# Kernel tuning notes

Hardware: AMD Instinct MI355X
Metric: run time of the kernel (lower is better)

The kernel has to match this reference:

```python
import jax, jax.numpy as jnp
import numpy as np

B, M, FIN, FOUT = 8, 2048, 256, 128
ALPHA = 0.2  # LeakyReLU negative slope
NEG_INF = -9e15


def _xavier_uniform(key, shape, gain):
    fan_in, fan_out = shape[0], shape[1]
    bound = gain * np.sqrt(6.0 / (fan_in + fan_out))
    return jax.random.uniform(key, shape, jnp.float32, -bound, bound)


def setup_inputs() -> dict:
    key = jax.random.key(0)
    k1, k2, k3, k4 = jax.random.split(key, 4)
    x = jax.random.normal(k1, (B, M, FIN), jnp.float32)
    adj1 = jax.random.randint(k2, (B, M, M), 0, 2).astype(jnp.int32)
    W = _xavier_uniform(k3, (FIN, FOUT), gain=2.0)
    a = _xavier_uniform(k4, (2 * FOUT, 1), gain=2.0)
    return {"input": x, "adj1": adj1, "W": W, "a": a}


def reference(input, adj1, W, a):
    # h: [B, M, FOUT]
    h = jnp.matmul(input, W)
    # e[b,i,j] = leakyrelu( concat(h_i, h_j) . a ) = leakyrelu( h_i.a1 + h_j.a2 )
    a1 = a[:FOUT, 0]   # [FOUT]
    a2 = a[FOUT:, 0]   # [FOUT]
    f1 = jnp.einsum('bme,e->bm', h, a1)  # source (row i) term
    f2 = jnp.einsum('bme,e->bm', h, a2)  # target (col j) term
    e = jax.nn.leaky_relu(f1[:, :, None] + f2[:, None, :], negative_slope=ALPHA)  # [B,M,M]
    scores = jnp.where(adj1 > 0, e, NEG_INF)
    attention = jax.nn.softmax(scores, axis=-1)
    # dropout is identity in eval mode (training=False)
    h_prime = jnp.matmul(attention, h)  # [B,M,FOUT]
    return jax.nn.elu(h_prime)  # concat=True branch
```

## Files before the change

### kernel.cpp

```cpp
#include <hip/hip_runtime.h>
#include <math.h>

#define B_    8
#define M_    2048
#define FIN_  256
#define FOUT_ 128
#define ALPHA_ 0.2f
#define NEG_INF_ -9.0e15f

typedef unsigned short u16;
typedef __attribute__((ext_vector_type(8))) short bf16x8;
typedef __attribute__((ext_vector_type(4))) float f32x4;

static __device__ __forceinline__ u16 f2bf(float f) {
  union { float f; unsigned u; } v; v.f = f;
  unsigned r = v.u + 0x7FFFu + ((v.u >> 16) & 1u);
  return (u16)(r >> 16);
}

__global__ __launch_bounds__(256) void k_wt(const float* __restrict__ W,
                                            u16* __restrict__ Wt) {
  const int id = blockIdx.x * 256 + threadIdx.x;
  const int f = id >> 8;
  const int k = id & 255;
  Wt[f * FIN_ + k] = f2bf(W[(size_t)k * FOUT_ + f]);
}

__global__ __launch_bounds__(128) void k_xw(const float* __restrict__ x,
                                            const u16* __restrict__ Wt,
                                            const float* __restrict__ a,
                                            u16* __restrict__ ht,
                                            float* __restrict__ f1,
                                            float* __restrict__ f2) {
  int blk = blockIdx.x;
  blk = (blk & 7) * 128 + (blk >> 3);
  const int b    = blk >> 7;
  const int row0 = (blk & 127) * 16;
  const int rowg = b * M_ + row0;
  const int tid  = threadIdx.x;
  const int w  = tid >> 6;
  const int l  = tid & 63;
  const int lr = l & 15;
  const int g  = l >> 4;
  const int fbase = w * 64;

  f32x4 acc[4];
#pragma unroll
  for (int ft = 0; ft < 4; ++ft) acc[ft] = (f32x4){0.f, 0.f, 0.f, 0.f};

  const float* xr = x + (size_t)(rowg + lr) * FIN_;
#pragma unroll
  for (int ks = 0; ks < 8; ++ks) {
    float4 xa = *(const float4*)(xr + ks * 32 + g * 8);
    float4 xc = *(const float4*)(xr + ks * 32 + g * 8 + 4);
    bf16x8 af;
    af[0] = (short)f2bf(xa.x); af[1] = (short)f2bf(xa.y);
    af[2] = (short)f2bf(xa.z); af[3] = (short)f2bf(xa.w);
    af[4] = (short)f2bf(xc.x); af[5] = (short)f2bf(xc.y);
    af[6] = (short)f2bf(xc.z); af[7] = (short)f2bf(xc.w);
#pragma unroll
    for (int ft = 0; ft < 4; ++ft) {
      bf16x8 bf = *(const bf16x8*)(Wt + (fbase + ft * 16 + lr) * FIN_ + ks * 32 + g * 8);
      acc[ft] = __builtin_amdgcn_mfma_f32_16x16x32_bf16(af, bf, acc[ft], 0, 0, 0);
    }
  }

  __shared__ float sf1[2][16], sf2[2][16];
  float v1[4] = {0.f, 0.f, 0.f, 0.f};
  float v2[4] = {0.f, 0.f, 0.f, 0.f};
#pragma unroll
  for (int ft = 0; ft < 4; ++ft) {
    const float a1v = a[fbase + ft * 16 + lr];
    const float a2v = a[FOUT_ + fbase + ft * 16 + lr];
#pragma unroll
    for (int j = 0; j < 4; ++j) {
      v1[j] += acc[ft][j] * a1v;
      v2[j] += acc[ft][j] * a2v;
    }
  }
#pragma unroll
  for (int off = 1; off < 16; off <<= 1) {
#pragma unroll
    for (int j = 0; j < 4; ++j) {
      v1[j] += __shfl_xor(v1[j], off);
      v2[j] += __shfl_xor(v2[j], off);
    }
  }
  if (lr == 0) {
#pragma unroll
    for (int j = 0; j < 4; ++j) {
      sf1[w][g * 4 + j] = v1[j];
      sf2[w][g * 4 + j] = v2[j];
    }
  }

  __shared__ float hs[16][132];
#pragma unroll
  for (int ft = 0; ft < 4; ++ft)
#pragma unroll
    for (int j = 0; j < 4; ++j)
      hs[g * 4 + j][fbase + ft * 16 + lr] = acc[ft][j];
  __syncthreads();

  if (tid < 16) {
    f1[rowg + tid] = sf1[0][tid] + sf1[1][tid];
    f2[rowg + tid] = sf2[0][tid] + sf2[1][tid];
  }
  const int f = tid;
  union { u16 u[16]; uint4 q[2]; } hb;
#pragma unroll
  for (int i = 0; i < 16; ++i) hb.u[i] = f2bf(hs[i][f]);
  u16* dst = ht + (size_t)(b * FOUT_ + f) * M_ + row0;
  *(uint4*)(dst)     = hb.q[0];
  *(uint4*)(dst + 8) = hb.q[1];
}

__global__ __launch_bounds__(256) void k_attn(const u16* __restrict__ ht,
                                              const int* __restrict__ adj,
                                              const float* __restrict__ f1,
                                              const float* __restrict__ f2,
                                              float* __restrict__ out) {
  int blk = blockIdx.x;
  blk = (blk & 7) * 128 + (blk >> 3);
  const int b    = blk >> 7;
  const int row0 = (blk & 127) * 16;
  const int tid = threadIdx.x;
  const int w  = tid >> 6;
  const int l  = tid & 63;
  const int lr = l & 15;
  const int g  = l >> 4;
  const int r  = tid >> 4;
  const int ts = tid & 15;

  __shared__ __align__(16) u16 P[2][16][128];
  __shared__ float sscale[2][16];
  __shared__ float smx[16], ssum[16], f1s[16];

  if (tid < 16) {
    smx[tid]  = -INFINITY;
    ssum[tid] = 0.f;
    f1s[tid]  = f1[b * M_ + row0 + tid];
  }

  f32x4 acc0 = (f32x4){0.f, 0.f, 0.f, 0.f};
  f32x4 acc1 = (f32x4){0.f, 0.f, 0.f, 0.f};

  const int fbase = w * 32;
  const int* ap   = adj + ((size_t)b * M_ + row0 + r) * M_ + ts * 8;
  const float* fp = f2 + b * M_ + ts * 8;
  const u16* hp0  = ht + (size_t)(b * FOUT_ + fbase + lr) * M_ + g * 8;
  const u16* hp1  = hp0 + 16 * M_;
  char* Pb = (char*)P;

  int4   ajA = *(const int4*)(ap);
  int4   ajB = *(const int4*)(ap + 4);
  float4 fvA = *(const float4*)(fp);
  float4 fvB = *(const float4*)(fp + 4);
  bf16x8 vbuf0[8], vbuf1[8];
#pragma unroll
  for (int ks = 0; ks < 4; ++ks) {
    vbuf0[ks]     = *(const bf16x8*)(hp0 + ks * 32);
    vbuf0[4 + ks] = *(const bf16x8*)(hp1 + ks * 32);
  }

  __syncthreads();

  auto iter = [&](int it, bf16x8 (&vcur)[8], bf16x8 (&vnxt)[8]) {
    const int n0 = it * 128;
    const int bi = it & 1;
    const int   aj[8] = {ajA.x, ajA.y, ajA.z, ajA.w, ajB.x, ajB.y, ajB.z, ajB.w};
    const float fv[8] = {fvA.x, fvA.y, fvA.z, fvA.w, fvB.x, fvB.y, fvB.z, fvB.w};
    const float f1r = f1s[r];
    float s[8];
#pragma unroll
    for (int i = 0; i < 8; ++i) {
      float z = f1r + fv[i];
      float e = z > 0.f ? z : ALPHA_ * z;
      s[i] = aj[i] > 0 ? e : NEG_INF_;
    }
    float cmax = s[0];
#pragma unroll
    for (int i = 1; i < 8; ++i) cmax = fmaxf(cmax, s[i]);
#pragma unroll
    for (int off = 1; off < 16; off <<= 1) cmax = fmaxf(cmax, __shfl_xor(cmax, off));
    const float m_old = smx[r];
    const float m_new = fmaxf(m_old, cmax);
    const float scl   = __expf(m_old - m_new);
    float psum = 0.f;
#pragma unroll
    for (int i = 0; i < 8; ++i) {
      float p = __expf(s[i] - m_new);
      s[i] = p;
      psum += p;
    }
#pragma unroll
    for (int off = 1; off < 16; off <<= 1) psum += __shfl_xor(psum, off);
    if (ts == 0) {
      smx[r]       = m_new;
      ssum[r]      = ssum[r] * scl + psum;
      sscale[bi][r] = scl;
    }
    union { u16 u[8]; uint4 q; } pw;
#pragma unroll
    for (int i = 0; i < 8; ++i) pw.u[i] = f2bf(s[i]);
    *(uint4*)(Pb + bi * 4096 + r * 256 + ((ts ^ (r & 7)) << 4)) = pw.q;
    __syncthreads();

    const int nn = (it + 1 < 16) ? (n0 + 128) : 0;
    ajA = *(const int4*)(ap + nn);
    ajB = *(const int4*)(ap + nn + 4);
    fvA = *(const float4*)(fp + nn);
    fvB = *(const float4*)(fp + nn + 4);
#pragma unroll
    for (int ks = 0; ks < 4; ++ks) {
      vnxt[ks]     = *(const bf16x8*)(hp0 + nn + ks * 32);
      vnxt[4 + ks] = *(const bf16x8*)(hp1 + nn + ks * 32);
    }
    f32x4 scv = { sscale[bi][g * 4],     sscale[bi][g * 4 + 1],
                  sscale[bi][g * 4 + 2], sscale[bi][g * 4 + 3] };
    acc0 *= scv;
    acc1 *= scv;
#pragma unroll
    for (int ks = 0; ks < 4; ++ks) {
      bf16x8 af = *(const bf16x8*)(Pb + bi * 4096 + lr * 256 +
                                   (((ks * 4 + g) ^ (lr & 7)) << 4));
      acc0 = __builtin_amdgcn_mfma_f32_16x16x32_bf16(af, vcur[ks],     acc0, 0, 0, 0);
      acc1 = __builtin_amdgcn_mfma_f32_16x16x32_bf16(af, vcur[4 + ks], acc1, 0, 0, 0);
    }
  };

#pragma unroll 1
  for (int it = 0; it < 16; it += 2) {
    iter(it,     vbuf0, vbuf1);
    iter(it + 1, vbuf1, vbuf0);
  }

  f32x4 inv = { 1.f / ssum[g * 4], 1.f / ssum[g * 4 + 1],
                1.f / ssum[g * 4 + 2], 1.f / ssum[g * 4 + 3] };
#pragma unroll
  for (int j = 0; j < 4; ++j) {
    const size_t orow = ((size_t)b * M_ + row0 + g * 4 + j) * FOUT_;
    float t0 = acc0[j] * inv[j];
    float t1 = acc1[j] * inv[j];
    out[orow + fbase + lr]      = t0 > 0.f ? t0 : __expf(t0) - 1.f;
    out[orow + fbase + 16 + lr] = t1 > 0.f ? t1 : __expf(t1) - 1.f;
  }
}

extern "C" void kernel_launch(void* const* d_in, const int* in_sizes, int n_in,
                              void* d_out, int out_size, void* d_ws, size_t ws_size,
                              hipStream_t stream) {
  const float* x   = (const float*)d_in[0];
  const int*   adj = (const int*)d_in[1];
  const float* W   = (const float*)d_in[2];
  const float* a   = (const float*)d_in[3];
  float* out = (float*)d_out;

  char* ws = (char*)d_ws;
  u16*   Wt = (u16*)ws;
  float* f1 = (float*)(ws + 65536);
  float* f2 = (float*)(ws + 131072);
  u16*   ht = (u16*)(ws + 196608);

  hipLaunchKernelGGL(k_wt,   dim3(128),  dim3(256), 0, stream, W, Wt);
  hipLaunchKernelGGL(k_xw,   dim3(1024), dim3(128), 0, stream, x, Wt, a, ht, f1, f2);
  hipLaunchKernelGGL(k_attn, dim3(1024), dim3(256), 0, stream, ht, adj, f1, f2, out);
}
```

Measured before the change: 259.3 us.

## Pack adjacency into bitmask in a pre-pass and read bits in attention

Adds a k_pack kernel that reads the int32 adjacency matrix once with coalesced loads and ballots each 64-column chunk into a 64-bit mask. The attention kernel then loads one 32-bit word per thread per tile instead of two int4 vectors, and tests bits to build the masked scores. The goal is to shrink the memory traffic and load latency inside the attention main loop. The cost is an extra kernel launch that still streams the full adjacency from memory, so total adjacency bytes read do not drop.

```diff
diff --git a/kernel.cpp b/kernel.cpp
--- a/kernel.cpp
+++ b/kernel.cpp
@@ -9,6 +9,8 @@
 #define NEG_INF_ -9.0e15f
 
 typedef unsigned short u16;
+typedef unsigned int   u32;
+typedef unsigned long long u64;
 typedef __attribute__((ext_vector_type(8))) short bf16x8;
 typedef __attribute__((ext_vector_type(4))) float f32x4;
 
@@ -24,6 +26,23 @@
   const int f = id >> 8;
   const int k = id & 255;
   Wt[f * FIN_ + k] = f2bf(W[(size_t)k * FOUT_ + f]);
+}
+
+__global__ __launch_bounds__(256) void k_pack(const int* __restrict__ adj,
+                                              u64* __restrict__ mask64) {
+  const int wid = (blockIdx.x * 256 + threadIdx.x) >> 6;
+  const int l   = threadIdx.x & 63;
+  const size_t base = (size_t)wid * 4096 + l;
+#pragma unroll 1
+  for (int kk = 0; kk < 4; ++kk) {
+#pragma unroll
+    for (int k = 0; k < 16; ++k) {
+      const int step = kk * 16 + k;
+      int v = adj[base + (size_t)step * 64];
+      u64 bal = __ballot(v > 0);
+      if (l == 0) mask64[(size_t)wid * 64 + step] = bal;
+    }
+  }
 }
 
 __global__ __launch_bounds__(128) void k_xw(const float* __restrict__ x,
@@ -116,7 +135,7 @@
 }
 
 __global__ __launch_bounds__(256) void k_attn(const u16* __restrict__ ht,
-                                              const int* __restrict__ adj,
+                                              const u32* __restrict__ mask32,
                                               const float* __restrict__ f1,
                                               const float* __restrict__ f2,
                                               float* __restrict__ out) {
@@ -146,14 +165,14 @@
   f32x4 acc1 = (f32x4){0.f, 0.f, 0.f, 0.f};
 
   const int fbase = w * 32;
-  const int* ap   = adj + ((size_t)b * M_ + row0 + r) * M_ + ts * 8;
+  const u32* mp   = mask32 + ((size_t)b * M_ + row0 + r) * 64 + (ts >> 2);
+  const int mshift = (ts & 3) * 8;
   const float* fp = f2 + b * M_ + ts * 8;
   const u16* hp0  = ht + (size_t)(b * FOUT_ + fbase + lr) * M_ + g * 8;
   const u16* hp1  = hp0 + 16 * M_;
   char* Pb = (char*)P;
 
-  int4   ajA = *(const int4*)(ap);
-  int4   ajB = *(const int4*)(ap + 4);
+  u32    mwA = mp[0];
   float4 fvA = *(const float4*)(fp);
   float4 fvB = *(const float4*)(fp + 4);
   bf16x8 vbuf0[8], vbuf1[8];
@@ -166,9 +185,8 @@
   __syncthreads();
 
   auto iter = [&](int it, bf16x8 (&vcur)[8], bf16x8 (&vnxt)[8]) {
-    const int n0 = it * 128;
     const int bi = it & 1;
-    const int   aj[8] = {ajA.x, ajA.y, ajA.z, ajA.w, ajB.x, ajB.y, ajB.z, ajB.w};
+    const u32   mbyte = (mwA >> mshift) & 0xffu;
     const float fv[8] = {fvA.x, fvA.y, fvA.z, fvA.w, fvB.x, fvB.y, fvB.z, fvB.w};
     const float f1r = f1s[r];
     float s[8];
@@ -176,7 +194,7 @@
     for (int i = 0; i < 8; ++i) {
       float z = f1r + fv[i];
       float e = z > 0.f ? z : ALPHA_ * z;
-      s[i] = aj[i] > 0 ? e : NEG_INF_;
+      s[i] = (mbyte & (1u << i)) ? e : NEG_INF_;
     }
     float cmax = s[0];
 #pragma unroll
@@ -196,8 +214,8 @@
 #pragma unroll
     for (int off = 1; off < 16; off <<= 1) psum += __shfl_xor(psum, off);
     if (ts == 0) {
-      smx[r]       = m_new;
-      ssum[r]      = ssum[r] * scl + psum;
+      smx[r]        = m_new;
+      ssum[r]       = ssum[r] * scl + psum;
       sscale[bi][r] = scl;
     }
     union { u16 u[8]; uint4 q; } pw;
@@ -206,15 +224,14 @@
     *(uint4*)(Pb + bi * 4096 + r * 256 + ((ts ^ (r & 7)) << 4)) = pw.q;
     __syncthreads();
 
-    const int nn = (it + 1 < 16) ? (n0 + 128) : 0;
-    ajA = *(const int4*)(ap + nn);
-    ajB = *(const int4*)(ap + nn + 4);
-    fvA = *(const float4*)(fp + nn);
-    fvB = *(const float4*)(fp + nn + 4);
+    const int itn = (it + 1 < 16) ? (it + 1) : 0;
+    mwA = mp[itn * 4];
+    fvA = *(const float4*)(fp + itn * 128);
+    fvB = *(const float4*)(fp + itn * 128 + 4);
 #pragma unroll
     for (int ks = 0; ks < 4; ++ks) {
-      vnxt[ks]     = *(const bf16x8*)(hp0 + nn + ks * 32);
-      vnxt[4 + ks] = *(const bf16x8*)(hp1 + nn + ks * 32);
+      vnxt[ks]     = *(const bf16x8*)(hp0 + itn * 128 + ks * 32);
+      vnxt[4 + ks] = *(const bf16x8*)(hp1 + itn * 128 + ks * 32);
     }
     f32x4 scv = { sscale[bi][g * 4],     sscale[bi][g * 4 + 1],
                   sscale[bi][g * 4 + 2], sscale[bi][g * 4 + 3] };
@@ -257,12 +274,14 @@
   float* out = (float*)d_out;
 
   char* ws = (char*)d_ws;
-  u16*   Wt = (u16*)ws;
-  float* f1 = (float*)(ws + 65536);
-  float* f2 = (float*)(ws + 131072);
-  u16*   ht = (u16*)(ws + 196608);
+  u16*   Wt   = (u16*)ws;
+  float* f1   = (float*)(ws + 65536);
+  float* f2   = (float*)(ws + 131072);
+  u16*   ht   = (u16*)(ws + 196608);
+  u64*   mask = (u64*)(ws + 196608 + 8388608);
 
   hipLaunchKernelGGL(k_wt,   dim3(128),  dim3(256), 0, stream, W, Wt);
+  hipLaunchKernelGGL(k_pack, dim3(2048), dim3(256), 0, stream, adj, mask);
   hipLaunchKernelGGL(k_xw,   dim3(1024), dim3(128), 0, stream, x, Wt, a, ht, f1, f2);
-  hipLaunchKernelGGL(k_attn, dim3(1024), dim3(256), 0, stream, ht, adj, f1, f2, out);
-}
+  hipLaunchKernelGGL(k_attn, dim3(1024), dim3(256), 0, stream, ht, (const u32*)mask, f1, f2, out);
+}
```

Measured after the change: 304.3 us. +17.4%, slower.

## Split attention columns across waves with register-resident P and lazy rescale

Applied to the files above, without the earlier changes.

Restructures the attention kernel so each of the four waves handles a quarter of the columns for all 16 rows and all 128 features. The probability tile is built directly in MFMA operand registers instead of passing through shared memory, which removes the per-iteration barrier. Accumulator rescaling is skipped unless the running max grows by more than a threshold, and the per-wave partial softmax states are merged through shared memory at the end. In exchange, each wave holds more accumulators and prefetch registers, and the merge adds a serialized reduction with several barriers.

```diff
diff --git a/kernel.cpp b/kernel.cpp
--- a/kernel.cpp
+++ b/kernel.cpp
@@ -9,6 +9,7 @@
 #define NEG_INF_ -9.0e15f
 
 typedef unsigned short u16;
+typedef unsigned int   u32;
 typedef __attribute__((ext_vector_type(8))) short bf16x8;
 typedef __attribute__((ext_vector_type(4))) float f32x4;
 
@@ -129,122 +130,131 @@
   const int l  = tid & 63;
   const int lr = l & 15;
   const int g  = l >> 4;
-  const int r  = tid >> 4;
-  const int ts = tid & 15;
-
-  __shared__ __align__(16) u16 P[2][16][128];
-  __shared__ float sscale[2][16];
-  __shared__ float smx[16], ssum[16], f1s[16];
-
-  if (tid < 16) {
-    smx[tid]  = -INFINITY;
-    ssum[tid] = 0.f;
-    f1s[tid]  = f1[b * M_ + row0 + tid];
-  }
-
-  f32x4 acc0 = (f32x4){0.f, 0.f, 0.f, 0.f};
-  f32x4 acc1 = (f32x4){0.f, 0.f, 0.f, 0.f};
-
-  const int fbase = w * 32;
-  const int* ap   = adj + ((size_t)b * M_ + row0 + r) * M_ + ts * 8;
-  const float* fp = f2 + b * M_ + ts * 8;
-  const u16* hp0  = ht + (size_t)(b * FOUT_ + fbase + lr) * M_ + g * 8;
-  const u16* hp1  = hp0 + 16 * M_;
-  char* Pb = (char*)P;
-
-  int4   ajA = *(const int4*)(ap);
-  int4   ajB = *(const int4*)(ap + 4);
-  float4 fvA = *(const float4*)(fp);
-  float4 fvB = *(const float4*)(fp + 4);
-  bf16x8 vbuf0[8], vbuf1[8];
-#pragma unroll
-  for (int ks = 0; ks < 4; ++ks) {
-    vbuf0[ks]     = *(const bf16x8*)(hp0 + ks * 32);
-    vbuf0[4 + ks] = *(const bf16x8*)(hp1 + ks * 32);
-  }
-
-  __syncthreads();
-
-  auto iter = [&](int it, bf16x8 (&vcur)[8], bf16x8 (&vnxt)[8]) {
-    const int n0 = it * 128;
-    const int bi = it & 1;
-    const int   aj[8] = {ajA.x, ajA.y, ajA.z, ajA.w, ajB.x, ajB.y, ajB.z, ajB.w};
+
+  const int colbase = w * 512;
+  const int*   ap = adj + ((size_t)(b * M_ + row0 + lr)) * M_ + colbase + g * 8;
+  const float* fp = f2 + b * M_ + colbase + g * 8;
+  const u16*   hp = ht + ((size_t)b * FOUT_ + lr) * M_ + colbase + g * 8;
+  const float f1r = f1[b * M_ + row0 + lr];
+
+  f32x4 acc[8];
+#pragma unroll
+  for (int ft = 0; ft < 8; ++ft) acc[ft] = (f32x4){0.f, 0.f, 0.f, 0.f};
+  float m = -INFINITY, lsum = 0.f;
+
+  int4   ajE0, ajE1, ajO0, ajO1;
+  float4 fA0, fA1, fB0, fB1;
+  bf16x8 vA[8], vB[8];
+
+  ajE0 = *(const int4*)(ap);       ajE1 = *(const int4*)(ap + 4);
+  ajO0 = *(const int4*)(ap + 32);  ajO1 = *(const int4*)(ap + 36);
+  fA0  = *(const float4*)(fp);     fA1  = *(const float4*)(fp + 4);
+#pragma unroll
+  for (int ft = 0; ft < 8; ++ft) vA[ft] = *(const bf16x8*)(hp + (size_t)ft * 16 * M_);
+
+  auto iter = [&](int c, int4& ajA, int4& ajB,
+                  float4& fvA, float4& fvB, bf16x8 (&vC)[8],
+                  float4& fnA, float4& fnB, bf16x8 (&vN)[8]) {
+    const int aj[8] = {ajA.x, ajA.y, ajA.z, ajA.w, ajB.x, ajB.y, ajB.z, ajB.w};
     const float fv[8] = {fvA.x, fvA.y, fvA.z, fvA.w, fvB.x, fvB.y, fvB.z, fvB.w};
-    const float f1r = f1s[r];
-    float s[8];
+    const int cn = (c + 1) & 15;
+    const int c2 = (c + 2) & 15;
+    fnA = *(const float4*)(fp + cn * 32);
+    fnB = *(const float4*)(fp + cn * 32 + 4);
+#pragma unroll
+    for (int ft = 0; ft < 8; ++ft)
+      vN[ft] = *(const bf16x8*)(hp + (size_t)ft * 16 * M_ + cn * 32);
+    ajA = *(const int4*)(ap + c2 * 32);
+    ajB = *(const int4*)(ap + c2 * 32 + 4);
+    float p[8];
+    float pmax = -INFINITY;
 #pragma unroll
     for (int i = 0; i < 8; ++i) {
       float z = f1r + fv[i];
       float e = z > 0.f ? z : ALPHA_ * z;
-      s[i] = aj[i] > 0 ? e : NEG_INF_;
-    }
-    float cmax = s[0];
-#pragma unroll
-    for (int i = 1; i < 8; ++i) cmax = fmaxf(cmax, s[i]);
-#pragma unroll
-    for (int off = 1; off < 16; off <<= 1) cmax = fmaxf(cmax, __shfl_xor(cmax, off));
-    const float m_old = smx[r];
-    const float m_new = fmaxf(m_old, cmax);
-    const float scl   = __expf(m_old - m_new);
+      float s = aj[i] > 0 ? e : NEG_INF_;
+      p[i] = s;
+      pmax = fmaxf(pmax, s);
+    }
+    pmax = fmaxf(pmax, __shfl_xor(pmax, 16));
+    pmax = fmaxf(pmax, __shfl_xor(pmax, 32));
+    if (!__all(pmax - m <= 8.f)) {
+      const float mnew = fmaxf(m, pmax);
+      const float scl  = __expf(m - mnew);
+      m = mnew;
+      lsum *= scl;
+      f32x4 sv = { __shfl(scl, g * 4 + 0), __shfl(scl, g * 4 + 1),
+                   __shfl(scl, g * 4 + 2), __shfl(scl, g * 4 + 3) };
+#pragma unroll
+      for (int ft = 0; ft < 8; ++ft) acc[ft] *= sv;
+    }
     float psum = 0.f;
+    bf16x8 af;
 #pragma unroll
     for (int i = 0; i < 8; ++i) {
-      float p = __expf(s[i] - m_new);
-      s[i] = p;
-      psum += p;
-    }
-#pragma unroll
-    for (int off = 1; off < 16; off <<= 1) psum += __shfl_xor(psum, off);
-    if (ts == 0) {
-      smx[r]       = m_new;
-      ssum[r]      = ssum[r] * scl + psum;
-      sscale[bi][r] = scl;
-    }
-    union { u16 u[8]; uint4 q; } pw;
-#pragma unroll
-    for (int i = 0; i < 8; ++i) pw.u[i] = f2bf(s[i]);
-    *(uint4*)(Pb + bi * 4096 + r * 256 + ((ts ^ (r & 7)) << 4)) = pw.q;
+      float pe = __expf(p[i] - m);
+      psum += pe;
+      af[i] = (short)f2bf(pe);
+    }
+    psum += __shfl_xor(psum, 16);
+    psum += __shfl_xor(psum, 32);
+    lsum += psum;
+#pragma unroll
+    for (int ft = 0; ft < 8; ++ft)
+      acc[ft] = __builtin_amdgcn_mfma_f32_16x16x32_bf16(af, vC[ft], acc[ft], 0, 0, 0);
+  };
+
+#pragma unroll 1
+  for (int cc = 0; cc < 16; cc += 2) {
+    iter(cc,     ajE0, ajE1, fA0, fA1, vA, fB0, fB1, vB);
+    iter(cc + 1, ajO0, ajO1, fB0, fB1, vB, fA0, fA1, vA);
+  }
+
+  __shared__ float sm[4][16], sl[4][16];
+  __shared__ float obuf[16][132];
+  if (l < 16) { sm[w][l] = m; sl[w][l] = lsum; }
+  __syncthreads();
+
+  f32x4 fac;
+#pragma unroll
+  for (int j = 0; j < 4; ++j) {
+    const int R = g * 4 + j;
+    const float M4 = fmaxf(fmaxf(sm[0][R], sm[1][R]), fmaxf(sm[2][R], sm[3][R]));
+    fac[j] = __expf(sm[w][R] - M4);
+  }
+#pragma unroll 1
+  for (int wk = 0; wk < 4; ++wk) {
+    if (w == wk) {
+#pragma unroll
+      for (int ft = 0; ft < 8; ++ft)
+#pragma unroll
+        for (int j = 0; j < 4; ++j) {
+          if (wk == 0) obuf[g * 4 + j][ft * 16 + lr]  = acc[ft][j] * fac[j];
+          else         obuf[g * 4 + j][ft * 16 + lr] += acc[ft][j] * fac[j];
+        }
+    }
     __syncthreads();
-
-    const int nn = (it + 1 < 16) ? (n0 + 128) : 0;
-    ajA = *(const int4*)(ap + nn);
-    ajB = *(const int4*)(ap + nn + 4);
-    fvA = *(const float4*)(fp + nn);
-    fvB = *(const float4*)(fp + nn + 4);
-#pragma unroll
-    for (int ks = 0; ks < 4; ++ks) {
-      vnxt[ks]     = *(const bf16x8*)(hp0 + nn + ks * 32);
-      vnxt[4 + ks] = *(const bf16x8*)(hp1 + nn + ks * 32);
-    }
-    f32x4 scv = { sscale[bi][g * 4],     sscale[bi][g * 4 + 1],
-                  sscale[bi][g * 4 + 2], sscale[bi][g * 4 + 3] };
-    acc0 *= scv;
-    acc1 *= scv;
-#pragma unroll
-    for (int ks = 0; ks < 4; ++ks) {
-      bf16x8 af = *(const bf16x8*)(Pb + bi * 4096 + lr * 256 +
-                                   (((ks * 4 + g) ^ (lr & 7)) << 4));
-      acc0 = __builtin_amdgcn_mfma_f32_16x16x32_bf16(af, vcur[ks],     acc0, 0, 0, 0);
-      acc1 = __builtin_amdgcn_mfma_f32_16x16x32_bf16(af, vcur[4 + ks], acc1, 0, 0, 0);
-    }
-  };
-
-#pragma unroll 1
-  for (int it = 0; it < 16; it += 2) {
-    iter(it,     vbuf0, vbuf1);
-    iter(it + 1, vbuf1, vbuf0);
-  }
-
-  f32x4 inv = { 1.f / ssum[g * 4], 1.f / ssum[g * 4 + 1],
-                1.f / ssum[g * 4 + 2], 1.f / ssum[g * 4 + 3] };
-#pragma unroll
-  for (int j = 0; j < 4; ++j) {
-    const size_t orow = ((size_t)b * M_ + row0 + g * 4 + j) * FOUT_;
-    float t0 = acc0[j] * inv[j];
-    float t1 = acc1[j] * inv[j];
-    out[orow + fbase + lr]      = t0 > 0.f ? t0 : __expf(t0) - 1.f;
-    out[orow + fbase + 16 + lr] = t1 > 0.f ? t1 : __expf(t1) - 1.f;
-  }
+  }
+
+  const int row = tid >> 4;
+  const int f0  = (tid & 15) * 8;
+  const float Mr = fmaxf(fmaxf(sm[0][row], sm[1][row]), fmaxf(sm[2][row], sm[3][row]));
+  const float Lr = sl[0][row] * __expf(sm[0][row] - Mr) + sl[1][row] * __expf(sm[1][row] - Mr)
+                 + sl[2][row] * __expf(sm[2][row] - Mr) + sl[3][row] * __expf(sm[3][row] - Mr);
+  const float inv = 1.0f / Lr;
+  float4 o0, o1;
+  float t;
+  t = obuf[row][f0 + 0] * inv; o0.x = t > 0.f ? t : __expf(t) - 1.f;
+  t = obuf[row][f0 + 1] * inv; o0.y = t > 0.f ? t : __expf(t) - 1.f;
+  t = obuf[row][f0 + 2] * inv; o0.z = t > 0.f ? t : __expf(t) - 1.f;
+  t = obuf[row][f0 + 3] * inv; o0.w = t > 0.f ? t : __expf(t) - 1.f;
+  t = obuf[row][f0 + 4] * inv; o1.x = t > 0.f ? t : __expf(t) - 1.f;
+  t = obuf[row][f0 + 5] * inv; o1.y = t > 0.f ? t : __expf(t) - 1.f;
+  t = obuf[row][f0 + 6] * inv; o1.z = t > 0.f ? t : __expf(t) - 1.f;
+  t = obuf[row][f0 + 7] * inv; o1.w = t > 0.f ? t : __expf(t) - 1.f;
+  float* op = out + ((size_t)b * M_ + row0 + row) * FOUT_ + f0;
+  *(float4*)(op)     = o0;
+  *(float4*)(op + 4) = o1;
 }
 
 extern "C" void kernel_launch(void* const* d_in, const int* in_sizes, int n_in,
```

New measurement: 290.8 us. 1.12x slower.
